# Performance work log

Hardware: AMD Instinct MI355X
Metric: run time of the kernel (lower is better)

Reference implementation:

```python
import jax, jax.numpy as jnp
import numpy as np

BOARDSIZE = 11
D = 512
H = 2
D_OBS = 7
D_POS = 18
P = BOARDSIZE * BOARDSIZE
OFFSETS = [(-1, 0), (-1, 1), (0, -1), (0, 0), (0, 1), (-1, -1), (-1, 0)]


def positions(boardsize):
    lin = jnp.linspace(-1.0, 1.0, boardsize)
    rs, cs = jnp.meshgrid(lin, lin, indexing='ij')
    zs = (rs + cs) / 2.0
    xs = jnp.stack([rs, cs, zs], -1)  # [bs, bs, 3]
    ps = [1, 2, 4]
    cos = jnp.concatenate([jnp.cos(2 * np.pi * xs / p) for p in ps], -1)
    sin = jnp.concatenate([jnp.sin(2 * np.pi * xs / p) for p in ps], -1)
    return jnp.concatenate([cos, sin], -1)  # [bs, bs, 18]


def _lin(x, W, b):
    return x @ W.T + b


def setup_inputs() -> dict:
    key = jax.random.key(0)
    ks = jax.random.split(key, 32)
    s = 0.02
    def W(k, o, i):
        return jax.random.normal(k, (o, i), jnp.float32) * s
    def bv(k, o):
        return jax.random.normal(k, (o,), jnp.float32) * s
    inp = {}
    inp['obs'] = jax.random.uniform(ks[0], (512, BOARDSIZE, BOARDSIZE, 2), jnp.float32)
    inp['W_first'] = W(ks[1], D, D);            inp['b_first'] = bv(ks[2], D)
    inp['W_kvx'] = W(ks[3], 2 * H * D, D);      inp['b_kvx'] = bv(ks[4], 2 * H * D)
    inp['W_kvb'] = W(ks[5], 2 * H * D, D_OBS + D_POS); inp['b_kvb'] = bv(ks[6], 2 * H * D)
    inp['W_q'] = W(ks[7], H * D, D);            inp['b_q'] = bv(ks[8], H * D)
    inp['W_fin'] = W(ks[9], D, H * D);          inp['b_fin'] = bv(ks[10], D)
    inp['W_sec'] = W(ks[11], D, D);             inp['b_sec'] = bv(ks[12], D)
    inp['W0_kp'] = W(ks[13], D, D_POS);         inp['b0_kp'] = bv(ks[14], D)
    inp['W0_kx'] = W(ks[15], D, D);             inp['b0_kx'] = bv(ks[16], D)
    inp['W0_q'] = W(ks[17], D, D);              inp['b0_q'] = bv(ks[18], D)
    inp['W1_kp'] = W(ks[19], D, D_POS);         inp['b1_kp'] = bv(ks[20], D)
    inp['W1_kx'] = W(ks[21], D, D);             inp['b1_kx'] = bv(ks[22], D)
    inp['W1_q'] = W(ks[23], D, D);              inp['b1_q'] = bv(ks[24], D)
    return inp


def _forward(obs, W_first, b_first, W_kvx, b_kvx, W_kvb, b_kvb, W_q, b_q,
             W_fin, b_fin, W_sec, b_sec,
             W0_kp, b0_kp, W0_kx, b0_kx, W0_q, b0_q,
             W1_kp, b1_kp, W1_kx, b1_kx, W1_q, b1_q):
    B = obs.shape[0]
    pos = positions(BOARDSIZE)  # [bs, bs, 18], constant
    # prepare: neighbourhoods + positional features
    single = obs[..., 0] - obs[..., 1]                      # [B, bs, bs]
    padded = jnp.pad(single, ((0, 0), (1, 1), (1, 1)))      # [B, bs+2, bs+2]
    nb = jnp.stack([padded[:, 1 + r:BOARDSIZE + 1 + r, 1 + c:BOARDSIZE + 1 + c]
                    for (r, c) in OFFSETS], -1)             # [B, bs, bs, 7]
    b = jnp.concatenate([nb, jnp.broadcast_to(pos, (B,) + pos.shape)], -1)
    b = b.reshape(B, P, D_OBS + D_POS)                      # [B, P, 25]
    # trunk
    x = jnp.zeros((B, D), obs.dtype)
    x = jax.nn.relu(_lin(x, W_first, b_first))
    # additive attention: kv = kv_x(x)[:,None] + kv_b(b)
    kv = _lin(x, W_kvx, b_kvx)[:, None, :] + _lin(b, W_kvb, b_kvb)  # [B, P, 4D]
    k, v = jnp.split(kv, 2, axis=-1)
    k = k.reshape(B, P, H, D)
    v = v.reshape(B, P, H, D)
    q = _lin(x, W_q, b_q).reshape(B, H, D)
    dots = jnp.einsum('bphd,bhd->bph', k, q) / np.sqrt(D)
    attn = jax.nn.softmax(dots, axis=1)                     # softmax over positions
    vals = jnp.einsum('bph,bphd->bhd', attn, v).reshape(B, H * D)
    x = _lin(vals, W_fin, b_fin)
    x = _lin(x, W_sec, b_sec)
    # policies (log-softmax over board positions)
    pflat = pos.reshape(P, D_POS)
    def policy(W_kp, b_kp, W_kx, b_kx, Wq, bq):
        kk = _lin(x, W_kx, b_kx)[:, None, :] + _lin(pflat, W_kp, b_kp)[None, :, :]
        qq = _lin(x, Wq, bq)
        d = jnp.einsum('bpd,bd->bp', kk, qq) / np.sqrt(D)
        return jax.nn.log_softmax(d, axis=-1).reshape(B, BOARDSIZE, BOARDSIZE)
    x0 = policy(W0_kp, b0_kp, W0_kx, b0_kx, W0_q, b0_q)
    x1 = policy(W1_kp, b1_kp, W1_kx, b1_kx, W1_q, b1_q)
    return x0, x1


def reference(obs, W_first, b_first, W_kvx, b_kvx, W_kvb, b_kvb, W_q, b_q,
              W_fin, b_fin, W_sec, b_sec,
              W0_kp, b0_kp, W0_kx, b0_kx, W0_q, b0_q,
              W1_kp, b1_kp, W1_kx, b1_kx, W1_q, b1_q):
    return _forward(obs, W_first, b_first, W_kvx, b_kvx, W_kvb, b_kvb, W_q, b_q,
                    W_fin, b_fin, W_sec, b_sec,
                    W0_kp, b0_kp, W0_kx, b0_kx, W0_q, b0_q,
                    W1_kp, b1_kp, W1_kx, b1_kx, W1_q, b1_q)
```

## Files before the change

kernel.cpp:

```cpp
#include <hip/hip_runtime.h>
#include <hip/hip_bf16.h>
#include <math.h>

#define NP 121
#define DD 512
#define INV_SQRT_D 0.04419417382415922f

#define O_X     0
#define O_KVX   512
#define O_QV    2560
#define O_POS   3584
#define O_W     5762
#define O_VC    5812
#define O_PC    6836
#define O_CFIN  7078
#define O_C2    7590
#define O_T1    8102
#define O_T2    33702
#define O_QC    59302
#define O_T3    60326
#define O_P     111526

__global__ void s1_pos_x(const float* __restrict__ b_first, float* __restrict__ ws) {
    int t = threadIdx.x;
    const float TWO_PI = 6.283185307179586f;
    for (int p = t; p < NP; p += blockDim.x) {
        int i = p / 11, j = p % 11;
        float r = (i - 5) * 0.2f, c = (j - 5) * 0.2f, z = 0.5f * (r + c);
        float xs[3] = {r, c, z};
        float pp[3] = {1.f, 2.f, 4.f};
        for (int a = 0; a < 3; a++)
            for (int q = 0; q < 3; q++) {
                float ang = TWO_PI * xs[q] / pp[a];
                ws[O_POS + p * 18 + a * 3 + q]     = cosf(ang);
                ws[O_POS + p * 18 + 9 + a * 3 + q] = sinf(ang);
            }
    }
    for (int d = t; d < DD; d += blockDim.x) ws[O_X + d] = fmaxf(b_first[d], 0.f);
}

__global__ void s2_kvx_qv(const float* __restrict__ W_kvx, const float* __restrict__ b_kvx,
                          const float* __restrict__ W_q, const float* __restrict__ b_q,
                          float* __restrict__ ws) {
    __shared__ float xs[DD];
    int t = threadIdx.x;
    for (int d = t; d < DD; d += 256) xs[d] = ws[O_X + d];
    __syncthreads();
    int wid = blockIdx.x * 4 + (t >> 6), lane = t & 63;
    const float* row; float bias; int outIdx;
    if (wid < 2048) { row = W_kvx + wid * DD; bias = b_kvx[wid]; outIdx = O_KVX + wid; }
    else { int r = wid - 2048; row = W_q + r * DD; bias = b_q[r]; outIdx = O_QV + r; }
    float acc = 0.f;
    for (int d = lane; d < DD; d += 64) acc += row[d] * xs[d];
    for (int o = 32; o; o >>= 1) acc += __shfl_xor(acc, o, 64);
    if (lane == 0) ws[outIdx] = acc + bias;
}

__global__ void s3_w_vc(const float* __restrict__ W_kvb, const float* __restrict__ b_kvb,
                        float* __restrict__ ws) {
    int blk = blockIdx.x, t = threadIdx.x;
    if (blk < 13) {
        int wv = blk * 4 + (t >> 6), lane = t & 63;
        if (wv < 50) {
            int h = wv / 25, j = wv % 25;
            float acc = 0.f;
            for (int d = lane; d < 512; d += 64)
                acc += W_kvb[(h * 512 + d) * 25 + j] * ws[O_QV + h * 512 + d];
            for (int o = 32; o; o >>= 1) acc += __shfl_xor(acc, o, 64);
            if (lane == 0) ws[O_W + wv] = acc;
        }
    } else {
        int idx = (blk - 13) * 256 + t;
        if (idx < 1024) ws[O_VC + idx] = ws[O_KVX + 1024 + idx] + b_kvb[1024 + idx];
    }
}

__device__ void gemm8x25(const float* __restrict__ A, int lda,
                         const float* __restrict__ B,
                         float* __restrict__ C, int nr) {
    __shared__ float Bl[256 * 25];
    __shared__ float Al[8 * 256];
    int t = threadIdx.x;
    int rl = t / 25, j = t - rl * 25;
    bool act = (t < 200) && (rl < nr);
    float acc = 0.f;
    for (int c = 0; c < 2; c++) {
        __syncthreads();
        for (int idx = t; idx < 6400; idx += 256) Bl[idx] = B[c * 6400 + idx];
        for (int idx = t; idx < 2048; idx += 256) {
            int rr = idx >> 8, dd = idx & 255;
            if (rr < nr) Al[idx] = A[rr * lda + c * 256 + dd];
        }
        __syncthreads();
        if (act) {
            const float* al = &Al[rl * 256];
            for (int dd = 0; dd < 256; dd++) acc += al[dd] * Bl[dd * 25 + j];
        }
    }
    if (act) C[rl * 25 + j] = acc;
}

__global__ void s4(const float* __restrict__ W_fin, const float* __restrict__ b_fin,
                   const float* __restrict__ W_kvb, float* __restrict__ ws) {
    int blk = blockIdx.x, t = threadIdx.x;
    if (blk < 128) {
        int row = blk * 4 + (t >> 6), lane = t & 63;
        float acc = 0.f;
        for (int d = lane; d < 1024; d += 64) acc += W_fin[row * 1024 + d] * ws[O_VC + d];
        for (int o = 32; o; o >>= 1) acc += __shfl_xor(acc, o, 64);
        if (lane == 0) ws[O_CFIN + row] = acc + b_fin[row];
    } else if (blk < 256) {
        int b2 = blk - 128, h = b2 >> 6, chunk = b2 & 63, r0 = chunk * 8;
        gemm8x25(W_fin + r0 * 1024 + h * 512, 1024,
                 W_kvb + (1024 + h * 512) * 25,
                 ws + O_T1 + (h * 512 + r0) * 25, 8);
    } else {
        if (t < 242) {
            int h = t / 121, p = t % 121;
            float acc = 0.f;
            for (int j = 0; j < 18; j++) acc += ws[O_W + h * 25 + 7 + j] * ws[O_POS + p * 18 + j];
            ws[O_PC + h * 121 + p] = acc;
        }
    }
}

__global__ void s5(const float* __restrict__ W_sec, const float* __restrict__ b_sec,
                   float* __restrict__ ws) {
    int blk = blockIdx.x, t = threadIdx.x;
    if (blk < 128) {
        int row = blk * 4 + (t >> 6), lane = t & 63;
        float acc = 0.f;
        for (int d = lane; d < 512; d += 64) acc += W_sec[row * 512 + d] * ws[O_CFIN + d];
        for (int o = 32; o; o >>= 1) acc += __shfl_xor(acc, o, 64);
        if (lane == 0) ws[O_C2 + row] = acc + b_sec[row];
    } else {
        int b2 = blk - 128, h = b2 >> 6, chunk = b2 & 63, r0 = chunk * 8;
        gemm8x25(W_sec + r0 * 512, 512,
                 ws + O_T1 + (h * 512) * 25,
                 ws + O_T2 + (h * 512 + r0) * 25, 8);
    }
}

__global__ void s6(const float* __restrict__ W0_q, const float* __restrict__ b0_q,
                   const float* __restrict__ W1_q, const float* __restrict__ b1_q,
                   float* __restrict__ ws) {
    int blk = blockIdx.x, t = threadIdx.x;
    if (blk < 256) {
        int row = blk * 4 + (t >> 6), lane = t & 63;
        int i = row >> 9, r = row & 511;
        const float* Wq = i ? W1_q : W0_q;
        const float* bq = i ? b1_q : b0_q;
        float acc = 0.f;
        for (int d = lane; d < 512; d += 64) acc += Wq[r * 512 + d] * ws[O_C2 + d];
        for (int o = 32; o; o >>= 1) acc += __shfl_xor(acc, o, 64);
        if (lane == 0) ws[O_QC + row] = acc + bq[r];
    } else {
        int b2 = blk - 256;
        int i = b2 >> 7, h = (b2 >> 6) & 1, chunk = b2 & 63, r0 = chunk * 8;
        const float* Wq = i ? W1_q : W0_q;
        gemm8x25(Wq + r0 * 512, 512,
                 ws + O_T2 + (h * 512) * 25,
                 ws + O_T3 + ((i * 2 + h) * 512 + r0) * 25, 8);
    }
}

__global__ void s7_fold(const float* __restrict__ W0_kp, const float* __restrict__ b0_kp,
                        const float* __restrict__ W1_kp, const float* __restrict__ b1_kp,
                        float* __restrict__ ws) {
    int gid = blockIdx.x * 4 + (threadIdx.x >> 6);
    int lane = threadIdx.x & 63;
    if (gid >= 1938) return;
    int i = gid / 969, rem = gid % 969, r = rem / 51, c = rem % 51;
    const float* kpW = i ? W1_kp : W0_kp;
    const float* kpb = i ? b1_kp : b0_kp;
    float acc = 0.f;
    for (int d = lane; d < 512; d += 64) {
        float kv = (r == 0) ? kpb[d] : kpW[d * 18 + (r - 1)];
        float gv;
        if (c == 0) gv = ws[O_QC + i * 512 + d];
        else {
            int h = (c - 1) / 25, f = (c - 1) % 25;
            gv = ws[O_T3 + ((i * 2 + h) * 512 + d) * 25 + f];
        }
        acc += kv * gv;
    }
    for (int o = 32; o; o >>= 1) acc += __shfl_xor(acc, o, 64);
    if (lane == 0) ws[O_P + gid] = acc;
}

__device__ __forceinline__ float blk_max2(float v, volatile float* tmp) {
    for (int o = 32; o; o >>= 1) v = fmaxf(v, __shfl_xor(v, o, 64));
    __syncthreads();
    if ((threadIdx.x & 63) == 0) tmp[threadIdx.x >> 6] = v;
    __syncthreads();
    return fmaxf(tmp[0], tmp[1]);
}
__device__ __forceinline__ float blk_sum2(float v, volatile float* tmp) {
    for (int o = 32; o; o >>= 1) v += __shfl_xor(v, o, 64);
    __syncthreads();
    if ((threadIdx.x & 63) == 0) tmp[threadIdx.x >> 6] = v;
    __syncthreads();
    return tmp[0] + tmp[1];
}

__global__ void s8_main(const float* __restrict__ obs, const float* __restrict__ ws,
                        float* __restrict__ out) {
    const int DRo[7] = {-1, -1, 0, 0, 0, -1, -1};
    const int DCo[7] = {0, 1, -1, 0, 1, -1, 0};
    __shared__ float sgl[121];
    __shared__ float nbs[121][7];
    __shared__ float att[121];
    __shared__ float bbar[2][25];
    __shared__ float g[51];
    __shared__ float cvec[19];
    __shared__ float tmp[2];
    int bid = blockIdx.x;
    int b = bid >> 1, pol = bid & 1;
    int t = threadIdx.x;
    if (t < 121) sgl[t] = obs[(b * 121 + t) * 2] - obs[(b * 121 + t) * 2 + 1];
    __syncthreads();
    float dots[2];
    if (t < 121) {
        int i = t / 11, j = t % 11;
        float nb[7];
        for (int k = 0; k < 7; k++) {
            int ii = i + DRo[k], jj = j + DCo[k];
            float v = (ii >= 0 && ii < 11 && jj >= 0 && jj < 11) ? sgl[ii * 11 + jj] : 0.f;
            nb[k] = v; nbs[t][k] = v;
        }
        for (int h = 0; h < 2; h++) {
            float acc = ws[O_PC + h * 121 + t];
            for (int k = 0; k < 7; k++) acc += ws[O_W + h * 25 + k] * nb[k];
            dots[h] = acc * INV_SQRT_D;
        }
    } else { dots[0] = dots[1] = -INFINITY; }
    for (int h = 0; h < 2; h++) {
        float m = blk_max2(dots[h], tmp);
        float e = (t < 121) ? expf(dots[h] - m) : 0.f;
        float s = blk_sum2(e, tmp);
        if (t < 121) att[t] = e / s;
        __syncthreads();
        if (t < 25) {
            float acc = 0.f;
            if (t < 7) { for (int p = 0; p < 121; p++) acc += att[p] * nbs[p][t]; }
            else { int j = t - 7; for (int p = 0; p < 121; p++) acc += att[p] * ws[O_POS + p * 18 + j]; }
            bbar[h][t] = acc;
        }
        __syncthreads();
    }
    if (t == 0) g[0] = 1.f;
    if (t < 50) g[1 + t] = bbar[t / 25][t % 25];
    __syncthreads();
    if (t < 19) {
        const float* Pr = ws + O_P + (pol * 19 + t) * 51;
        float a = 0.f;
        for (int c = 0; c < 51; c++) a += Pr[c] * g[c];
        cvec[t] = a;
    }
    __syncthreads();
    float d;
    if (t < 121) {
        d = cvec[0];
        for (int j = 0; j < 18; j++) d += ws[O_POS + t * 18 + j] * cvec[1 + j];
        d *= INV_SQRT_D;
    } else d = -INFINITY;
    float m = blk_max2(d, tmp);
    float e = (t < 121) ? expf(d - m) : 0.f;
    float s = blk_sum2(e, tmp);
    float ls = logf(s);
    if (t < 121) out[pol * 61952 + b * 121 + t] = d - m - ls;
}

extern "C" void kernel_launch(void* const* d_in, const int* in_sizes, int n_in,
                              void* d_out, int out_size, void* d_ws, size_t ws_size,
                              hipStream_t stream) {
    const float* obs     = (const float*)d_in[0];
    const float* b_first = (const float*)d_in[2];
    const float* W_kvx   = (const float*)d_in[3];
    const float* b_kvx   = (const float*)d_in[4];
    const float* W_kvb   = (const float*)d_in[5];
    const float* b_kvb   = (const float*)d_in[6];
    const float* W_q     = (const float*)d_in[7];
    const float* b_q     = (const float*)d_in[8];
    const float* W_fin   = (const float*)d_in[9];
    const float* b_fin   = (const float*)d_in[10];
    const float* W_sec   = (const float*)d_in[11];
    const float* b_sec   = (const float*)d_in[12];
    const float* W0_kp   = (const float*)d_in[13];
    const float* b0_kp   = (const float*)d_in[14];
    const float* W0_q    = (const float*)d_in[17];
    const float* b0_q    = (const float*)d_in[18];
    const float* W1_kp   = (const float*)d_in[19];
    const float* b1_kp   = (const float*)d_in[20];
    const float* W1_q    = (const float*)d_in[23];
    const float* b1_q    = (const float*)d_in[24];
    float* ws = (float*)d_ws;
    float* out = (float*)d_out;

    hipLaunchKernelGGL(s1_pos_x, dim3(1),   dim3(256), 0, stream, b_first, ws);
    hipLaunchKernelGGL(s2_kvx_qv, dim3(768), dim3(256), 0, stream, W_kvx, b_kvx, W_q, b_q, ws);
    hipLaunchKernelGGL(s3_w_vc, dim3(17), dim3(256), 0, stream, W_kvb, b_kvb, ws);
    hipLaunchKernelGGL(s4, dim3(257), dim3(256), 0, stream, W_fin, b_fin, W_kvb, ws);
    hipLaunchKernelGGL(s5, dim3(256), dim3(256), 0, stream, W_sec, b_sec, ws);
    hipLaunchKernelGGL(s6, dim3(512), dim3(256), 0, stream, W0_q, b0_q, W1_q, b1_q, ws);
    hipLaunchKernelGGL(s7_fold, dim3(485), dim3(256), 0, stream, W0_kp, b0_kp, W1_kp, b1_kp, ws);
    hipLaunchKernelGGL(s8_main, dim3(1024), dim3(128), 0, stream, obs, ws, out);
}
```

Before: 169.9 us.

## Fuse all stages into one persistent kernel with software grid barriers

Replaces eight separate kernel launches with a single 512-block persistent kernel that uses atomic-counter grid barriers between phases. It also reschedules the stages so independent work overlaps: the first folded GEMM runs alongside the kvx/q projections and position encoding, and the bias fold into the policy term is recomputed per batch block. The main gain sought is removing launch and inter-kernel gaps. The risks are deadlock if not all 512 blocks are co-resident, barrier spin overhead, and redundant per-block recomputation of the kp/qc column.

```diff
diff --git a/kernel.cpp b/kernel.cpp
--- a/kernel.cpp
+++ b/kernel.cpp
@@ -1,95 +1,52 @@
 #include <hip/hip_runtime.h>
-#include <hip/hip_bf16.h>
 #include <math.h>
 
-#define NP 121
-#define DD 512
+#define NBLK 512
+#define NTHR 256
 #define INV_SQRT_D 0.04419417382415922f
 
-#define O_X     0
-#define O_KVX   512
-#define O_QV    2560
-#define O_POS   3584
-#define O_W     5762
-#define O_VC    5812
-#define O_PC    6836
-#define O_CFIN  7078
-#define O_C2    7590
-#define O_T1    8102
-#define O_T2    33702
-#define O_QC    59302
-#define O_T3    60326
-#define O_P     111526
-
-__global__ void s1_pos_x(const float* __restrict__ b_first, float* __restrict__ ws) {
-    int t = threadIdx.x;
-    const float TWO_PI = 6.283185307179586f;
-    for (int p = t; p < NP; p += blockDim.x) {
-        int i = p / 11, j = p % 11;
-        float r = (i - 5) * 0.2f, c = (j - 5) * 0.2f, z = 0.5f * (r + c);
-        float xs[3] = {r, c, z};
-        float pp[3] = {1.f, 2.f, 4.f};
-        for (int a = 0; a < 3; a++)
-            for (int q = 0; q < 3; q++) {
-                float ang = TWO_PI * xs[q] / pp[a];
-                ws[O_POS + p * 18 + a * 3 + q]     = cosf(ang);
-                ws[O_POS + p * 18 + 9 + a * 3 + q] = sinf(ang);
-            }
-    }
-    for (int d = t; d < DD; d += blockDim.x) ws[O_X + d] = fmaxf(b_first[d], 0.f);
-}
-
-__global__ void s2_kvx_qv(const float* __restrict__ W_kvx, const float* __restrict__ b_kvx,
-                          const float* __restrict__ W_q, const float* __restrict__ b_q,
-                          float* __restrict__ ws) {
-    __shared__ float xs[DD];
-    int t = threadIdx.x;
-    for (int d = t; d < DD; d += 256) xs[d] = ws[O_X + d];
-    __syncthreads();
-    int wid = blockIdx.x * 4 + (t >> 6), lane = t & 63;
-    const float* row; float bias; int outIdx;
-    if (wid < 2048) { row = W_kvx + wid * DD; bias = b_kvx[wid]; outIdx = O_KVX + wid; }
-    else { int r = wid - 2048; row = W_q + r * DD; bias = b_q[r]; outIdx = O_QV + r; }
-    float acc = 0.f;
-    for (int d = lane; d < DD; d += 64) acc += row[d] * xs[d];
-    for (int o = 32; o; o >>= 1) acc += __shfl_xor(acc, o, 64);
-    if (lane == 0) ws[outIdx] = acc + bias;
-}
-
-__global__ void s3_w_vc(const float* __restrict__ W_kvb, const float* __restrict__ b_kvb,
-                        float* __restrict__ ws) {
-    int blk = blockIdx.x, t = threadIdx.x;
-    if (blk < 13) {
-        int wv = blk * 4 + (t >> 6), lane = t & 63;
-        if (wv < 50) {
-            int h = wv / 25, j = wv % 25;
-            float acc = 0.f;
-            for (int d = lane; d < 512; d += 64)
-                acc += W_kvb[(h * 512 + d) * 25 + j] * ws[O_QV + h * 512 + d];
-            for (int o = 32; o; o >>= 1) acc += __shfl_xor(acc, o, 64);
-            if (lane == 0) ws[O_W + wv] = acc;
-        }
-    } else {
-        int idx = (blk - 13) * 256 + t;
-        if (idx < 1024) ws[O_VC + idx] = ws[O_KVX + 1024 + idx] + b_kvb[1024 + idx];
-    }
-}
-
-__device__ void gemm8x25(const float* __restrict__ A, int lda,
-                         const float* __restrict__ B,
-                         float* __restrict__ C, int nr) {
-    __shared__ float Bl[256 * 25];
-    __shared__ float Al[8 * 256];
+#define O_POS   0
+#define O_KVXV  2178
+#define O_QV    3202
+#define O_W     4226
+#define O_PC    4276
+#define O_CFIN  4518
+#define O_C2    5030
+#define O_T1    5542
+#define O_T2    31142
+#define O_QC    56742
+#define O_T3    57766
+#define O_P     108966
+#define O_BAR   110912
+
+#define MAGIC 0x5ca1ab1eu
+
+__device__ __forceinline__ void gridbar(unsigned* bar, int phase) {
+    __syncthreads();
+    if (threadIdx.x == 0) {
+        __hip_atomic_fetch_add(&bar[1 + phase], 1u, __ATOMIC_ACQ_REL, __HIP_MEMORY_SCOPE_AGENT);
+        long long spins = 0;
+        while (__hip_atomic_load(&bar[1 + phase], __ATOMIC_ACQUIRE, __HIP_MEMORY_SCOPE_AGENT) < (unsigned)NBLK) {
+            if (++spins > 200000000LL) break;
+        }
+    }
+    __syncthreads();
+}
+
+__device__ void gemm8x25(float* sh, const float* __restrict__ A, int lda,
+                         const float* __restrict__ B, float* __restrict__ C) {
+    float* Bl = sh;
+    float* Al = sh + 6400;
     int t = threadIdx.x;
     int rl = t / 25, j = t - rl * 25;
-    bool act = (t < 200) && (rl < nr);
+    bool act = (t < 200);
     float acc = 0.f;
     for (int c = 0; c < 2; c++) {
         __syncthreads();
         for (int idx = t; idx < 6400; idx += 256) Bl[idx] = B[c * 6400 + idx];
         for (int idx = t; idx < 2048; idx += 256) {
             int rr = idx >> 8, dd = idx & 255;
-            if (rr < nr) Al[idx] = A[rr * lda + c * 256 + dd];
+            Al[idx] = A[rr * lda + c * 256 + dd];
         }
         __syncthreads();
         if (act) {
@@ -100,175 +57,235 @@
     if (act) C[rl * 25 + j] = acc;
 }
 
-__global__ void s4(const float* __restrict__ W_fin, const float* __restrict__ b_fin,
-                   const float* __restrict__ W_kvb, float* __restrict__ ws) {
-    int blk = blockIdx.x, t = threadIdx.x;
+__device__ __forceinline__ float blkmax(float v, volatile float* tmp) {
+    for (int o = 32; o; o >>= 1) v = fmaxf(v, __shfl_xor(v, o, 64));
+    __syncthreads();
+    if ((threadIdx.x & 63) == 0) tmp[threadIdx.x >> 6] = v;
+    __syncthreads();
+    float r = fmaxf(fmaxf(tmp[0], tmp[1]), fmaxf(tmp[2], tmp[3]));
+    __syncthreads();
+    return r;
+}
+__device__ __forceinline__ float blksum(float v, volatile float* tmp) {
+    for (int o = 32; o; o >>= 1) v += __shfl_xor(v, o, 64);
+    __syncthreads();
+    if ((threadIdx.x & 63) == 0) tmp[threadIdx.x >> 6] = v;
+    __syncthreads();
+    float r = tmp[0] + tmp[1] + tmp[2] + tmp[3];
+    __syncthreads();
+    return r;
+}
+
+__global__ __launch_bounds__(NTHR, 4) void mega(
+    const float* __restrict__ obs, const float* __restrict__ b_first,
+    const float* __restrict__ W_kvx, const float* __restrict__ b_kvx,
+    const float* __restrict__ W_kvb, const float* __restrict__ b_kvb,
+    const float* __restrict__ W_q, const float* __restrict__ b_q,
+    const float* __restrict__ W_fin, const float* __restrict__ b_fin,
+    const float* __restrict__ W_sec, const float* __restrict__ b_sec,
+    const float* __restrict__ W0_kp, const float* __restrict__ b0_kp,
+    const float* __restrict__ W0_q, const float* __restrict__ b0_q,
+    const float* __restrict__ W1_kp, const float* __restrict__ b1_kp,
+    const float* __restrict__ W1_q, const float* __restrict__ b1_q,
+    float* __restrict__ ws, float* __restrict__ out)
+{
+    __shared__ float sh[8448];
+    unsigned* bar = (unsigned*)(ws + O_BAR);
+    int blk = blockIdx.x, t = threadIdx.x, wv = t >> 6, lane = t & 63;
+
+    if (blk == 0) {
+        if (t < 8) __hip_atomic_store(&bar[1 + t], 0u, __ATOMIC_RELAXED, __HIP_MEMORY_SCOPE_AGENT);
+        __syncthreads();
+        if (t == 0) __hip_atomic_store(&bar[0], MAGIC, __ATOMIC_RELEASE, __HIP_MEMORY_SCOPE_AGENT);
+    } else {
+        if (t == 0) {
+            long long spins = 0;
+            while (__hip_atomic_load(&bar[0], __ATOMIC_ACQUIRE, __HIP_MEMORY_SCOPE_AGENT) != MAGIC)
+                if (++spins > 200000000LL) break;
+        }
+        __syncthreads();
+    }
+
     if (blk < 128) {
-        int row = blk * 4 + (t >> 6), lane = t & 63;
-        float acc = 0.f;
-        for (int d = lane; d < 1024; d += 64) acc += W_fin[row * 1024 + d] * ws[O_VC + d];
-        for (int o = 32; o; o >>= 1) acc += __shfl_xor(acc, o, 64);
-        if (lane == 0) ws[O_CFIN + row] = acc + b_fin[row];
-    } else if (blk < 256) {
-        int b2 = blk - 128, h = b2 >> 6, chunk = b2 & 63, r0 = chunk * 8;
-        gemm8x25(W_fin + r0 * 1024 + h * 512, 1024,
-                 W_kvb + (1024 + h * 512) * 25,
-                 ws + O_T1 + (h * 512 + r0) * 25, 8);
-    } else {
+        int h = blk >> 6, chunk = blk & 63, r0 = chunk * 8;
+        gemm8x25(sh, W_fin + r0 * 1024 + h * 512, 1024,
+                 W_kvb + (1024 + h * 512) * 25, ws + O_T1 + (h * 512 + r0) * 25);
+    } else if (blk < 384) {
+        for (int k = 0; k < 2; k++) {
+            int row = (blk - 128) * 8 + wv * 2 + k;
+            const float* R; float bias; int oi;
+            if (row < 1024) { R = W_kvx + (1024 + row) * 512; bias = b_kvx[1024 + row]; oi = O_KVXV + row; }
+            else { int r2 = row - 1024; R = W_q + r2 * 512; bias = b_q[r2]; oi = O_QV + r2; }
+            float a = 0.f;
+            for (int d = lane; d < 512; d += 64) a += R[d] * fmaxf(b_first[d], 0.f);
+            for (int o = 32; o; o >>= 1) a += __shfl_xor(a, o, 64);
+            if (lane == 0) ws[oi] = a + bias;
+        }
+    } else if (blk < 393) {
+        int gid = (blk - 384) * 256 + t;
+        if (gid < 2178) {
+            int p = gid / 18, jj = gid % 18;
+            int i = p / 11, j = p % 11;
+            float r = (i - 5) * 0.2f, c = (j - 5) * 0.2f, z = 0.5f * (r + c);
+            float xs3[3] = {r, c, z};
+            float pp3[3] = {1.f, 2.f, 4.f};
+            int sc = jj / 9, rem = jj % 9, a = rem / 3, q = rem % 3;
+            float ang = 6.283185307179586f * xs3[q] / pp3[a];
+            ws[O_POS + p * 18 + jj] = sc ? sinf(ang) : cosf(ang);
+        }
+    }
+    gridbar(bar, 0);
+
+    if (blk < 128) {
+        int h = blk >> 6, chunk = blk & 63, r0 = chunk * 8;
+        gemm8x25(sh, W_sec + r0 * 512, 512,
+                 ws + O_T1 + h * 512 * 25, ws + O_T2 + (h * 512 + r0) * 25);
+    } else if (blk < 141) {
+        int wid = (blk - 128) * 4 + wv;
+        if (wid < 50) {
+            int h = wid / 25, j = wid % 25;
+            float a = 0.f;
+            for (int d = lane; d < 512; d += 64) a += W_kvb[(h * 512 + d) * 25 + j] * ws[O_QV + h * 512 + d];
+            for (int o = 32; o; o >>= 1) a += __shfl_xor(a, o, 64);
+            if (lane == 0) ws[O_W + wid] = a;
+        }
+    } else if (blk < 269) {
+        int row = (blk - 141) * 4 + wv;
+        float a = 0.f;
+        for (int d = lane; d < 1024; d += 64) a += W_fin[row * 1024 + d] * (ws[O_KVXV + d] + b_kvb[1024 + d]);
+        for (int o = 32; o; o >>= 1) a += __shfl_xor(a, o, 64);
+        if (lane == 0) ws[O_CFIN + row] = a + b_fin[row];
+    }
+    gridbar(bar, 1);
+
+    if (blk < 256) {
+        int i = blk >> 7, h = (blk >> 6) & 1, chunk = blk & 63, r0 = chunk * 8;
+        const float* Wq = i ? W1_q : W0_q;
+        gemm8x25(sh, Wq + r0 * 512, 512,
+                 ws + O_T2 + h * 512 * 25, ws + O_T3 + ((i * 2 + h) * 512 + r0) * 25);
+    } else if (blk < 384) {
+        int row = (blk - 256) * 4 + wv;
+        float a = 0.f;
+        for (int d = lane; d < 512; d += 64) a += W_sec[row * 512 + d] * ws[O_CFIN + d];
+        for (int o = 32; o; o >>= 1) a += __shfl_xor(a, o, 64);
+        if (lane == 0) ws[O_C2 + row] = a + b_sec[row];
+    } else if (blk == 384) {
         if (t < 242) {
             int h = t / 121, p = t % 121;
-            float acc = 0.f;
-            for (int j = 0; j < 18; j++) acc += ws[O_W + h * 25 + 7 + j] * ws[O_POS + p * 18 + j];
-            ws[O_PC + h * 121 + p] = acc;
-        }
-    }
-}
-
-__global__ void s5(const float* __restrict__ W_sec, const float* __restrict__ b_sec,
-                   float* __restrict__ ws) {
-    int blk = blockIdx.x, t = threadIdx.x;
-    if (blk < 128) {
-        int row = blk * 4 + (t >> 6), lane = t & 63;
-        float acc = 0.f;
-        for (int d = lane; d < 512; d += 64) acc += W_sec[row * 512 + d] * ws[O_CFIN + d];
-        for (int o = 32; o; o >>= 1) acc += __shfl_xor(acc, o, 64);
-        if (lane == 0) ws[O_C2 + row] = acc + b_sec[row];
-    } else {
-        int b2 = blk - 128, h = b2 >> 6, chunk = b2 & 63, r0 = chunk * 8;
-        gemm8x25(W_sec + r0 * 512, 512,
-                 ws + O_T1 + (h * 512) * 25,
-                 ws + O_T2 + (h * 512 + r0) * 25, 8);
-    }
-}
-
-__global__ void s6(const float* __restrict__ W0_q, const float* __restrict__ b0_q,
-                   const float* __restrict__ W1_q, const float* __restrict__ b1_q,
-                   float* __restrict__ ws) {
-    int blk = blockIdx.x, t = threadIdx.x;
+            float a = 0.f;
+            for (int j = 0; j < 18; j++) a += ws[O_W + h * 25 + 7 + j] * ws[O_POS + p * 18 + j];
+            ws[O_PC + h * 121 + p] = a;
+        }
+    }
+    gridbar(bar, 2);
+
     if (blk < 256) {
-        int row = blk * 4 + (t >> 6), lane = t & 63;
-        int i = row >> 9, r = row & 511;
+        int row = blk * 4 + wv, i = row >> 9, r = row & 511;
         const float* Wq = i ? W1_q : W0_q;
         const float* bq = i ? b1_q : b0_q;
-        float acc = 0.f;
-        for (int d = lane; d < 512; d += 64) acc += Wq[r * 512 + d] * ws[O_C2 + d];
-        for (int o = 32; o; o >>= 1) acc += __shfl_xor(acc, o, 64);
-        if (lane == 0) ws[O_QC + row] = acc + bq[r];
-    } else {
-        int b2 = blk - 256;
-        int i = b2 >> 7, h = (b2 >> 6) & 1, chunk = b2 & 63, r0 = chunk * 8;
-        const float* Wq = i ? W1_q : W0_q;
-        gemm8x25(Wq + r0 * 512, 512,
-                 ws + O_T2 + (h * 512) * 25,
-                 ws + O_T3 + ((i * 2 + h) * 512 + r0) * 25, 8);
-    }
-}
-
-__global__ void s7_fold(const float* __restrict__ W0_kp, const float* __restrict__ b0_kp,
-                        const float* __restrict__ W1_kp, const float* __restrict__ b1_kp,
-                        float* __restrict__ ws) {
-    int gid = blockIdx.x * 4 + (threadIdx.x >> 6);
-    int lane = threadIdx.x & 63;
-    if (gid >= 1938) return;
-    int i = gid / 969, rem = gid % 969, r = rem / 51, c = rem % 51;
-    const float* kpW = i ? W1_kp : W0_kp;
-    const float* kpb = i ? b1_kp : b0_kp;
-    float acc = 0.f;
-    for (int d = lane; d < 512; d += 64) {
-        float kv = (r == 0) ? kpb[d] : kpW[d * 18 + (r - 1)];
-        float gv;
-        if (c == 0) gv = ws[O_QC + i * 512 + d];
-        else {
-            int h = (c - 1) / 25, f = (c - 1) % 25;
-            gv = ws[O_T3 + ((i * 2 + h) * 512 + d) * 25 + f];
-        }
-        acc += kv * gv;
-    }
-    for (int o = 32; o; o >>= 1) acc += __shfl_xor(acc, o, 64);
-    if (lane == 0) ws[O_P + gid] = acc;
-}
-
-__device__ __forceinline__ float blk_max2(float v, volatile float* tmp) {
-    for (int o = 32; o; o >>= 1) v = fmaxf(v, __shfl_xor(v, o, 64));
-    __syncthreads();
-    if ((threadIdx.x & 63) == 0) tmp[threadIdx.x >> 6] = v;
-    __syncthreads();
-    return fmaxf(tmp[0], tmp[1]);
-}
-__device__ __forceinline__ float blk_sum2(float v, volatile float* tmp) {
-    for (int o = 32; o; o >>= 1) v += __shfl_xor(v, o, 64);
-    __syncthreads();
-    if ((threadIdx.x & 63) == 0) tmp[threadIdx.x >> 6] = v;
-    __syncthreads();
-    return tmp[0] + tmp[1];
-}
-
-__global__ void s8_main(const float* __restrict__ obs, const float* __restrict__ ws,
-                        float* __restrict__ out) {
-    const int DRo[7] = {-1, -1, 0, 0, 0, -1, -1};
-    const int DCo[7] = {0, 1, -1, 0, 1, -1, 0};
-    __shared__ float sgl[121];
-    __shared__ float nbs[121][7];
-    __shared__ float att[121];
-    __shared__ float bbar[2][25];
-    __shared__ float g[51];
-    __shared__ float cvec[19];
-    __shared__ float tmp[2];
-    int bid = blockIdx.x;
-    int b = bid >> 1, pol = bid & 1;
-    int t = threadIdx.x;
-    if (t < 121) sgl[t] = obs[(b * 121 + t) * 2] - obs[(b * 121 + t) * 2 + 1];
-    __syncthreads();
-    float dots[2];
-    if (t < 121) {
-        int i = t / 11, j = t % 11;
-        float nb[7];
-        for (int k = 0; k < 7; k++) {
-            int ii = i + DRo[k], jj = j + DCo[k];
-            float v = (ii >= 0 && ii < 11 && jj >= 0 && jj < 11) ? sgl[ii * 11 + jj] : 0.f;
-            nb[k] = v; nbs[t][k] = v;
-        }
+        float a = 0.f;
+        for (int d = lane; d < 512; d += 64) a += Wq[r * 512 + d] * ws[O_C2 + d];
+        for (int o = 32; o; o >>= 1) a += __shfl_xor(a, o, 64);
+        if (lane == 0) ws[O_QC + row] = a + bq[r];
+    } else if (blk < 506) {
+        int wid = (blk - 256) * 4 + wv;
+        for (int rep = 0; rep < 2; rep++) {
+            int D = wid * 2 + rep;
+            if (D < 1900) {
+                int i = D / 950, rem = D % 950, r = rem / 50, c1 = rem % 50;
+                int h = c1 / 25, f = c1 % 25;
+                const float* kpW = i ? W1_kp : W0_kp;
+                const float* kpb = i ? b1_kp : b0_kp;
+                float a = 0.f;
+                for (int d = lane; d < 512; d += 64) {
+                    float kv = (r == 0) ? kpb[d] : kpW[d * 18 + (r - 1)];
+                    a += kv * ws[O_T3 + ((i * 2 + h) * 512 + d) * 25 + f];
+                }
+                for (int o = 32; o; o >>= 1) a += __shfl_xor(a, o, 64);
+                if (lane == 0) ws[O_P + i * 969 + r * 51 + (1 + c1)] = a;
+            }
+        }
+    }
+    gridbar(bar, 3);
+
+    {
+        float* sgl  = sh;
+        float* nbs  = sh + 128;
+        float* att  = sh + 1024;
+        float* bbar = sh + 1152;
+        float* colp = sh + 1202;
+        float* cvec = sh + 1356;
+        float* tmp  = sh + 1376;
+        int b = blk;
+        if (t < 121) sgl[t] = obs[(b * 121 + t) * 2] - obs[(b * 121 + t) * 2 + 1];
+        __syncthreads();
+        float dots[2];
+        if (t < 121) {
+            const int DRo[7] = {-1, -1, 0, 0, 0, -1, -1};
+            const int DCo[7] = {0, 1, -1, 0, 1, -1, 0};
+            int i = t / 11, j = t % 11;
+            float nb[7];
+            for (int k = 0; k < 7; k++) {
+                int ii = i + DRo[k], jj = j + DCo[k];
+                float v = (ii >= 0 && ii < 11 && jj >= 0 && jj < 11) ? sgl[ii * 11 + jj] : 0.f;
+                nb[k] = v; nbs[t * 7 + k] = v;
+            }
+            for (int h = 0; h < 2; h++) {
+                float acc = ws[O_PC + h * 121 + t];
+                for (int k = 0; k < 7; k++) acc += ws[O_W + h * 25 + k] * nb[k];
+                dots[h] = acc * INV_SQRT_D;
+            }
+        } else { dots[0] = dots[1] = -INFINITY; }
         for (int h = 0; h < 2; h++) {
-            float acc = ws[O_PC + h * 121 + t];
-            for (int k = 0; k < 7; k++) acc += ws[O_W + h * 25 + k] * nb[k];
-            dots[h] = acc * INV_SQRT_D;
-        }
-    } else { dots[0] = dots[1] = -INFINITY; }
-    for (int h = 0; h < 2; h++) {
-        float m = blk_max2(dots[h], tmp);
-        float e = (t < 121) ? expf(dots[h] - m) : 0.f;
-        float s = blk_sum2(e, tmp);
-        if (t < 121) att[t] = e / s;
-        __syncthreads();
-        if (t < 25) {
-            float acc = 0.f;
-            if (t < 7) { for (int p = 0; p < 121; p++) acc += att[p] * nbs[p][t]; }
-            else { int j = t - 7; for (int p = 0; p < 121; p++) acc += att[p] * ws[O_POS + p * 18 + j]; }
-            bbar[h][t] = acc;
-        }
-        __syncthreads();
-    }
-    if (t == 0) g[0] = 1.f;
-    if (t < 50) g[1 + t] = bbar[t / 25][t % 25];
-    __syncthreads();
-    if (t < 19) {
-        const float* Pr = ws + O_P + (pol * 19 + t) * 51;
-        float a = 0.f;
-        for (int c = 0; c < 51; c++) a += Pr[c] * g[c];
-        cvec[t] = a;
-    }
-    __syncthreads();
-    float d;
-    if (t < 121) {
-        d = cvec[0];
-        for (int j = 0; j < 18; j++) d += ws[O_POS + t * 18 + j] * cvec[1 + j];
-        d *= INV_SQRT_D;
-    } else d = -INFINITY;
-    float m = blk_max2(d, tmp);
-    float e = (t < 121) ? expf(d - m) : 0.f;
-    float s = blk_sum2(e, tmp);
-    float ls = logf(s);
-    if (t < 121) out[pol * 61952 + b * 121 + t] = d - m - ls;
+            float m = blkmax(dots[h], tmp);
+            float e = (t < 121) ? expf(dots[h] - m) : 0.f;
+            float s = blksum(e, tmp);
+            if (t < 121) att[t] = e / s;
+            __syncthreads();
+            if (t < 25) {
+                float acc = 0.f;
+                if (t < 7) { for (int p = 0; p < 121; p++) acc += att[p] * nbs[p * 7 + t]; }
+                else { int j = t - 7; for (int p = 0; p < 121; p++) acc += att[p] * ws[O_POS + p * 18 + j]; }
+                bbar[h * 25 + t] = acc;
+            }
+            __syncthreads();
+        }
+        for (int pol = 0; pol < 2; pol++) {
+            const float* kpW = pol ? W1_kp : W0_kp;
+            const float* kpb = pol ? b1_kp : b0_kp;
+            if (t < 152) {
+                int r = t >> 3, sgm = t & 7;
+                const float* qcp = ws + O_QC + pol * 512;
+                float a = 0.f;
+                for (int d = sgm * 64; d < sgm * 64 + 64; d++) {
+                    float kv = (r == 0) ? kpb[d] : kpW[d * 18 + (r - 1)];
+                    a += kv * qcp[d];
+                }
+                colp[r * 8 + sgm] = a;
+            }
+            __syncthreads();
+            if (t < 19) {
+                float a = 0.f;
+                for (int s = 0; s < 8; s++) a += colp[t * 8 + s];
+                const float* Pr = ws + O_P + pol * 969 + t * 51;
+                for (int c = 1; c < 51; c++) a += Pr[c] * bbar[c - 1];
+                cvec[t] = a;
+            }
+            __syncthreads();
+            float d;
+            if (t < 121) {
+                d = cvec[0];
+                for (int j = 0; j < 18; j++) d += ws[O_POS + t * 18 + j] * cvec[1 + j];
+                d *= INV_SQRT_D;
+            } else d = -INFINITY;
+            float m = blkmax(d, tmp);
+            float e = (t < 121) ? expf(d - m) : 0.f;
+            float s = blksum(e, tmp);
+            float ls = logf(s);
+            if (t < 121) out[pol * 61952 + b * 121 + t] = d - m - ls;
+            __syncthreads();
+        }
+    }
 }
 
 extern "C" void kernel_launch(void* const* d_in, const int* in_sizes, int n_in,
@@ -297,12 +314,9 @@
     float* ws = (float*)d_ws;
     float* out = (float*)d_out;
 
-    hipLaunchKernelGGL(s1_pos_x, dim3(1),   dim3(256), 0, stream, b_first, ws);
-    hipLaunchKernelGGL(s2_kvx_qv, dim3(768), dim3(256), 0, stream, W_kvx, b_kvx, W_q, b_q, ws);
-    hipLaunchKernelGGL(s3_w_vc, dim3(17), dim3(256), 0, stream, W_kvb, b_kvb, ws);
-    hipLaunchKernelGGL(s4, dim3(257), dim3(256), 0, stream, W_fin, b_fin, W_kvb, ws);
-    hipLaunchKernelGGL(s5, dim3(256), dim3(256), 0, stream, W_sec, b_sec, ws);
-    hipLaunchKernelGGL(s6, dim3(512), dim3(256), 0, stream, W0_q, b0_q, W1_q, b1_q, ws);
-    hipLaunchKernelGGL(s7_fold, dim3(485), dim3(256), 0, stream, W0_kp, b0_kp, W1_kp, b1_kp, ws);
-    hipLaunchKernelGGL(s8_main, dim3(1024), dim3(128), 0, stream, obs, ws, out);
-}
+    hipLaunchKernelGGL(mega, dim3(NBLK), dim3(NTHR), 0, stream,
+                       obs, b_first, W_kvx, b_kvx, W_kvb, b_kvb, W_q, b_q,
+                       W_fin, b_fin, W_sec, b_sec,
+                       W0_kp, b0_kp, W0_q, b0_q, W1_kp, b1_kp, W1_q, b1_q,
+                       ws, out);
+}
```

New measurement: 456.4 us. +168.6%, slower.
